# Kernel optimization log

Hardware: AMD Instinct MI355X
Metric: run time of the kernel (lower is better)

The kernel has to match this reference:

```python
import jax, jax.numpy as jnp
import numpy as np

EPS = 1e-5

def layer_norm(x, gamma, beta):
    mu = jnp.mean(x, axis=-1, keepdims=True)
    var = jnp.mean(jnp.square(x - mu), axis=-1, keepdims=True)
    return (x - mu) * jax.lax.rsqrt(var + EPS) * gamma + beta

def setup_inputs() -> dict:
    key = jax.random.key(0)
    ks = jax.random.split(key, 16)
    B, Cq, Hq, Wq = 8, 256, 32, 32
    Cc, Hc, Wc = 512, 64, 64
    def lin(k, fan_in, fan_out):
        lim = 1.0 / np.sqrt(fan_in)
        k1, k2 = jax.random.split(k)
        W = jax.random.uniform(k1, (fan_in, fan_out), jnp.float32, -lim, lim)
        b = jax.random.uniform(k2, (fan_out,), jnp.float32, -lim, lim)
        return W, b
    Wq_, bq = lin(ks[0], Cq, Cq)
    Wk_, bk = lin(ks[1], Cc, Cq)
    Wv_, bv = lin(ks[2], Cc, Cq)
    Wo_, bo = lin(ks[3], Cq, Cq)
    return {
        "query": jax.random.normal(ks[4], (B, Cq, Hq, Wq), jnp.float32),
        "context": jax.random.normal(ks[5], (B, Cc, Hc, Wc), jnp.float32),
        "Wq": Wq_, "bq": bq, "Wk": Wk_, "bk": bk, "Wv": Wv_, "bv": bv,
        "Wo": Wo_, "bo": bo,
        "gq": jnp.ones((Cq,), jnp.float32), "betq": jnp.zeros((Cq,), jnp.float32),
        "gc": jnp.ones((Cc,), jnp.float32), "betc": jnp.zeros((Cc,), jnp.float32),
    }

def reference(query, context, Wq, bq, Wk, bk, Wv, bv, Wo, bo, gq, betq, gc, betc):
    B, Cq, Hq, Wq_sp = query.shape
    _, Cc, Hc, Wc = context.shape
    num_heads = 8
    head_dim = Cq // num_heads
    scale = jnp.sqrt(jnp.float32(head_dim))
    N = Hq * Wq_sp
    # adaptive_avg_pool2d with divisible sizes == average pooling over equal bins
    ctx = context.reshape(B, Cc, Hq, Hc // Hq, Wq_sp, Wc // Wq_sp).mean(axis=(3, 5))
    q_flat = query.reshape(B, Cq, N).transpose(0, 2, 1)          # (B,N,Cq)
    c_flat = ctx.reshape(B, Cc, N).transpose(0, 2, 1)            # (B,N,Cc)
    qn = layer_norm(q_flat, gq, betq)
    cn = layer_norm(c_flat, gc, betc)
    q = (qn @ Wq + bq).reshape(B, N, num_heads, head_dim).transpose(0, 2, 1, 3)
    k = (cn @ Wk + bk).reshape(B, N, num_heads, head_dim).transpose(0, 2, 1, 3)
    v = (cn @ Wv + bv).reshape(B, N, num_heads, head_dim).transpose(0, 2, 1, 3)
    attn = jnp.einsum('bhnd,bhmd->bhnm', q, k) / scale
    attn = jax.nn.softmax(attn, axis=-1)
    out = jnp.einsum('bhnm,bhmd->bhnd', attn, v)
    out = out.transpose(0, 2, 1, 3).reshape(B, N, Cq)
    out = out @ Wo + bo
    out = q_flat + out                                           # residual
    return out.transpose(0, 2, 1).reshape(B, Cq, Hq, Wq_sp)
```

## Files before the change

kernel.cpp:

```cpp
#include <hip/hip_runtime.h>
#include <hip/hip_bf16.h>
#include <cstddef>

#define B_  8
#define CQ  256
#define CC  512
#define N_  1024
#define HQ  32
#define WQ  32
#define NH  8
#define HD  32

typedef __bf16 bf16x8 __attribute__((ext_vector_type(8)));
typedef float f32x4 __attribute__((ext_vector_type(4)));
typedef float f32x16 __attribute__((ext_vector_type(16)));
typedef unsigned int uint4v __attribute__((ext_vector_type(4)));
typedef unsigned short ushort8 __attribute__((ext_vector_type(8)));
typedef unsigned short ushort4v __attribute__((ext_vector_type(4)));

__device__ __forceinline__ unsigned short f2bf(float x) {
    return __builtin_bit_cast(unsigned short, __float2bfloat16(x));
}
__device__ __forceinline__ bf16x8 ldb8(const unsigned short* p) {
    return __builtin_bit_cast(bf16x8, *(const ushort8*)p);
}

__global__ __launch_bounds__(256) void prep_k(
    const float* __restrict__ query, const float* __restrict__ context,
    const float* __restrict__ Wq, const float* __restrict__ Wk,
    const float* __restrict__ Wv, const float* __restrict__ Wo,
    const float* __restrict__ gq, const float* __restrict__ betq,
    const float* __restrict__ gc, const float* __restrict__ betc,
    __hip_bfloat16* __restrict__ Wqt, __hip_bfloat16* __restrict__ Wkt,
    __hip_bfloat16* __restrict__ Wvt, __hip_bfloat16* __restrict__ Wot,
    __hip_bfloat16* __restrict__ qn, __hip_bfloat16* __restrict__ cn) {
    __shared__ float T[32][33];
    __shared__ float SsA[64][16];
    __shared__ float S2A[64][16];
    __shared__ float SsB[16][64];
    __shared__ float S2B[16][64];
    __shared__ float Mu[64], Rs[64];

    const int bid = blockIdx.x;
    const int tid = threadIdx.x;

    if (bid < 512) {
        const int x = bid & 15, y = (bid >> 4) & 7, z = bid >> 7;
        const float* W; __hip_bfloat16* Wt; int K;
        switch (z) {
            case 0: W = Wq; Wt = Wqt; K = CQ; break;
            case 1: W = Wk; Wt = Wkt; K = CC; break;
            case 2: W = Wv; Wt = Wvt; K = CC; break;
            default: W = Wo; Wt = Wot; K = CQ; break;
        }
        const int k0 = x * 32;
        if (k0 >= K) return;
        const int c0 = y * 32;
        const int tx = tid & 31, ty = tid >> 5;
        #pragma unroll
        for (int i = 0; i < 4; ++i) {
            const int r = ty + 8 * i;
            T[r][tx] = W[(size_t)(k0 + r) * CQ + c0 + tx];
        }
        __syncthreads();
        #pragma unroll
        for (int i = 0; i < 4; ++i) {
            const int r = ty + 8 * i;
            Wt[(size_t)(c0 + r) * K + k0 + tx] = __float2bfloat16(T[tx][r]);
        }
    } else if (bid < 1536) {
        const int u   = bid - 512;
        const int wq8 = u & 3, hq = (u >> 2) & 31, b = u >> 7;
        const int pp  = tid & 3;
        const int cg  = tid >> 2;
        const int ch0 = cg * 8;

        const float* Cb = context + ((size_t)b * CC + ch0) * 4096
                        + (size_t)(2 * hq) * 64 + (16 * wq8 + 4 * pp);
        float pv0[8], pv1[8];
        float ss0 = 0.f, ss1 = 0.f, s20 = 0.f, s21 = 0.f;
        #pragma unroll
        for (int i = 0; i < 8; ++i) {
            const float4 r0 = *(const float4*)(Cb + (size_t)i * 4096);
            const float4 r1 = *(const float4*)(Cb + (size_t)i * 4096 + 64);
            const float v0 = (r0.x + r0.y + r1.x + r1.y) * 0.25f;
            const float v1 = (r0.z + r0.w + r1.z + r1.w) * 0.25f;
            pv0[i] = v0; pv1[i] = v1;
            ss0 += v0; s20 += v0 * v0;
            ss1 += v1; s21 += v1 * v1;
        }
        SsA[cg][2 * pp]     = ss0; S2A[cg][2 * pp]     = s20;
        SsA[cg][2 * pp + 1] = ss1; S2A[cg][2 * pp + 1] = s21;
        __syncthreads();
        if (tid < 8) {
            float ts = 0.f, t2 = 0.f;
            #pragma unroll
            for (int i = 0; i < 64; ++i) { ts += SsA[i][tid]; t2 += S2A[i][tid]; }
            const float mu  = ts * (1.f / CC);
            const float var = t2 * (1.f / CC) - mu * mu;
            Mu[tid] = mu; Rs[tid] = rsqrtf(var + 1e-5f);
        }
        __syncthreads();
        const float mu0 = Mu[2 * pp],     rs0 = Rs[2 * pp];
        const float mu1 = Mu[2 * pp + 1], rs1 = Rs[2 * pp + 1];
        const int pos = hq * 32 + wq8 * 8 + 2 * pp;
        unsigned short* dst = (unsigned short*)cn
            + ((size_t)b * N_ + pos) * CC + ch0;
        ushort8 o0, o1;
        #pragma unroll
        for (int e = 0; e < 8; ++e) {
            o0[e] = f2bf((pv0[e] - mu0) * rs0 * gc[ch0 + e] + betc[ch0 + e]);
            o1[e] = f2bf((pv1[e] - mu1) * rs1 * gc[ch0 + e] + betc[ch0 + e]);
        }
        *(ushort8*)(dst)      = o0;
        *(ushort8*)(dst + CC) = o1;
    } else {
        const int u  = bid - 1536;
        const int nt = u & 15, b = u >> 4;
        const int nq = tid & 15;
        const int cg = tid >> 4;
        const int ch0 = cg * 16;
        const int nb  = nt * 64 + 4 * nq;

        const float* Qb = query + ((size_t)b * CQ + ch0) * N_ + nb;
        float qv[64];
        float ps[4] = {0.f, 0.f, 0.f, 0.f};
        float p2[4] = {0.f, 0.f, 0.f, 0.f};
        #pragma unroll
        for (int i = 0; i < 16; ++i) {
            const float4 v = *(const float4*)(Qb + (size_t)i * N_);
            qv[4 * i + 0] = v.x; qv[4 * i + 1] = v.y;
            qv[4 * i + 2] = v.z; qv[4 * i + 3] = v.w;
            ps[0] += v.x; p2[0] += v.x * v.x;
            ps[1] += v.y; p2[1] += v.y * v.y;
            ps[2] += v.z; p2[2] += v.z * v.z;
            ps[3] += v.w; p2[3] += v.w * v.w;
        }
        #pragma unroll
        for (int j = 0; j < 4; ++j) {
            SsB[cg][4 * nq + j] = ps[j];
            S2B[cg][4 * nq + j] = p2[j];
        }
        __syncthreads();
        if (tid < 64) {
            float ts = 0.f, t2 = 0.f;
            #pragma unroll
            for (int i = 0; i < 16; ++i) { ts += SsB[i][tid]; t2 += S2B[i][tid]; }
            const float mu  = ts * (1.f / CQ);
            const float var = t2 * (1.f / CQ) - mu * mu;
            Mu[tid] = mu; Rs[tid] = rsqrtf(var + 1e-5f);
        }
        __syncthreads();
        #pragma unroll
        for (int j = 0; j < 4; ++j) {
            const float mu = Mu[4 * nq + j], rs = Rs[4 * nq + j];
            ushort8 o0, o1;
            #pragma unroll
            for (int i = 0; i < 8; ++i)
                o0[i] = f2bf((qv[4 * i + j] - mu) * rs * gq[ch0 + i] + betq[ch0 + i]);
            #pragma unroll
            for (int i = 0; i < 8; ++i)
                o1[i] = f2bf((qv[4 * (8 + i) + j] - mu) * rs * gq[ch0 + 8 + i] + betq[ch0 + 8 + i]);
            unsigned short* dst = (unsigned short*)qn
                + ((size_t)b * N_ + nb + j) * CQ + ch0;
            *(ushort8*)(dst)     = o0;
            *(ushort8*)(dst + 8) = o1;
        }
    }
}

__global__ __launch_bounds__(256) void proj_all_k(
    const __hip_bfloat16* __restrict__ qn, const __hip_bfloat16* __restrict__ cn,
    const __hip_bfloat16* __restrict__ Wqt, const __hip_bfloat16* __restrict__ Wkt,
    const __hip_bfloat16* __restrict__ Wvt,
    const float* __restrict__ bq, const float* __restrict__ bk,
    const float* __restrict__ bv,
    __hip_bfloat16* __restrict__ Qb, __hip_bfloat16* __restrict__ Kb,
    __hip_bfloat16* __restrict__ Vt, float qsc) {
    __shared__ unsigned short As[64][40];
    __shared__ unsigned short B1[64][40];
    __shared__ unsigned short B2[64][40];

    const int zz = blockIdx.z;
    const int n0 = blockIdx.x * 64;
    const int c0 = blockIdx.y * 64;
    const int tid = threadIdx.x;
    const int wid = tid >> 6, lane = tid & 63;
    const int lg = lane >> 4, ln = lane & 15;
    const int wn0 = (wid & 1) * 32, wc0 = (wid >> 1) * 32;
    const int sr = tid >> 2;
    const int sk = (tid & 3) * 8;

    if (zz >= 8) {
        const int b = zz - 8;
        const unsigned short* Ab = (const unsigned short*)qn + ((size_t)b * N_ + n0) * CQ;
        const unsigned short* Wb = (const unsigned short*)Wqt + (size_t)c0 * CQ;
        f32x4 acc[2][2] = {};
        ushort8 ra = *(const ushort8*)(Ab + (size_t)sr * CQ + sk);
        ushort8 rw = *(const ushort8*)(Wb + (size_t)sr * CQ + sk);
        for (int t = 0; t < 8; ++t) {
            *(ushort8*)&As[sr][sk] = ra;
            *(ushort8*)&B1[sr][sk] = rw;
            __syncthreads();
            if (t < 7) {
                ra = *(const ushort8*)(Ab + (size_t)sr * CQ + (t + 1) * 32 + sk);
                rw = *(const ushort8*)(Wb + (size_t)sr * CQ + (t + 1) * 32 + sk);
            }
            bf16x8 a[2], w[2];
            #pragma unroll
            for (int i = 0; i < 2; ++i) a[i] = ldb8(&As[wn0 + 16 * i + ln][8 * lg]);
            #pragma unroll
            for (int j = 0; j < 2; ++j) w[j] = ldb8(&B1[wc0 + 16 * j + ln][8 * lg]);
            #pragma unroll
            for (int i = 0; i < 2; ++i)
                #pragma unroll
                for (int j = 0; j < 2; ++j)
                    acc[i][j] = __builtin_amdgcn_mfma_f32_16x16x32_bf16(a[i], w[j], acc[i][j], 0, 0, 0);
            __syncthreads();
        }
        #pragma unroll
        for (int j = 0; j < 2; ++j) {
            const int co = c0 + wc0 + 16 * j + ln;
            const int h = co >> 5, d = co & 31;
            const float bb = bq[co];
            #pragma unroll
            for (int i = 0; i < 2; ++i)
                #pragma unroll
                for (int r = 0; r < 4; ++r) {
                    const int n = n0 + wn0 + 16 * i + 4 * lg + r;
                    Qb[(((size_t)b * NH + h) * N_ + n) * HD + d] =
                        __float2bfloat16((acc[i][j][r] + bb) * qsc);
                }
        }
    } else {
        const int b = zz;
        const unsigned short* Ab  = (const unsigned short*)cn + ((size_t)b * N_ + n0) * CC;
        const unsigned short* Wkb = (const unsigned short*)Wkt + (size_t)c0 * CC;
        const unsigned short* Wvb = (const unsigned short*)Wvt + (size_t)c0 * CC;
        f32x4 accK[2][2] = {};
        f32x4 accV[2][2] = {};
        ushort8 ra = *(const ushort8*)(Ab  + (size_t)sr * CC + sk);
        ushort8 rk = *(const ushort8*)(Wkb + (size_t)sr * CC + sk);
        ushort8 rv = *(const ushort8*)(Wvb + (size_t)sr * CC + sk);
        for (int t = 0; t < 16; ++t) {
            *(ushort8*)&As[sr][sk] = ra;
            *(ushort8*)&B1[sr][sk] = rk;
            *(ushort8*)&B2[sr][sk] = rv;
            __syncthreads();
            if (t < 15) {
                ra = *(const ushort8*)(Ab  + (size_t)sr * CC + (t + 1) * 32 + sk);
                rk = *(const ushort8*)(Wkb + (size_t)sr * CC + (t + 1) * 32 + sk);
                rv = *(const ushort8*)(Wvb + (size_t)sr * CC + (t + 1) * 32 + sk);
            }
            bf16x8 a[2], wk[2], wv[2];
            #pragma unroll
            for (int i = 0; i < 2; ++i) {
                a[i]  = ldb8(&As[wn0 + 16 * i + ln][8 * lg]);
                wk[i] = ldb8(&B1[wc0 + 16 * i + ln][8 * lg]);
                wv[i] = ldb8(&B2[wc0 + 16 * i + ln][8 * lg]);
            }
            #pragma unroll
            for (int i = 0; i < 2; ++i)
                #pragma unroll
                for (int j = 0; j < 2; ++j) {
                    accK[i][j] = __builtin_amdgcn_mfma_f32_16x16x32_bf16(a[i], wk[j], accK[i][j], 0, 0, 0);
                    accV[i][j] = __builtin_amdgcn_mfma_f32_16x16x32_bf16(a[i], wv[j], accV[i][j], 0, 0, 0);
                }
            __syncthreads();
        }
        #pragma unroll
        for (int j = 0; j < 2; ++j) {
            const int co = c0 + wc0 + 16 * j + ln;
            const int h = co >> 5, d = co & 31;
            const float bbk = bk[co], bbv = bv[co];
            #pragma unroll
            for (int i = 0; i < 2; ++i) {
                const int nb = n0 + wn0 + 16 * i + 4 * lg;
                #pragma unroll
                for (int r = 0; r < 4; ++r)
                    Kb[(((size_t)b * NH + h) * N_ + nb + r) * HD + d] =
                        __float2bfloat16(accK[i][j][r] + bbk);
                ushort4v o;
                #pragma unroll
                for (int r = 0; r < 4; ++r) o[r] = f2bf(accV[i][j][r] + bbv);
                const int g  = (nb >> 2) & 3;
                const int gp = ((g & 1) << 1) | (g >> 1);
                const int nbp = (nb & ~15) | (gp << 2);
                *(ushort4v*)((unsigned short*)Vt + (((size_t)b * NH + h) * HD + d) * N_ + nbp) = o;
            }
        }
    }
}

__global__ __launch_bounds__(256) void attn32_k(
    const __hip_bfloat16* __restrict__ Q,
    const __hip_bfloat16* __restrict__ K,
    const __hip_bfloat16* __restrict__ Vt,
    __hip_bfloat16* __restrict__ O) {
    __shared__ float accS[3][64][20];
    __shared__ float lwS[3][64];

    const int lin = blockIdx.x + 32 * blockIdx.y;
    const int eff = (lin & 7) * 256 + (lin >> 3);
    const int qt  = eff & 31;
    const int bh  = eff >> 5;
    const int b   = bh >> 3;
    const int h   = bh & 7;
    const int wid  = threadIdx.x >> 6;
    const int lane = threadIdx.x & 63;
    const int l31  = lane & 31;
    const int hh   = lane >> 5;
    const int q0   = qt * 32;

    const unsigned short* Qp = (const unsigned short*)Q + ((size_t)bh * N_ + q0) * HD;
    const unsigned short* Kbb = (const unsigned short*)K + (size_t)bh * N_ * HD;
    const unsigned short* Vb = (const unsigned short*)Vt + ((size_t)bh * HD + l31) * N_;

    bf16x8 qB[2];
    #pragma unroll
    for (int m = 0; m < 2; ++m)
        qB[m] = ldb8(Qp + (size_t)l31 * HD + 16 * m + 8 * hh);

    const f32x16 Z = {0.f,0.f,0.f,0.f,0.f,0.f,0.f,0.f,
                      0.f,0.f,0.f,0.f,0.f,0.f,0.f,0.f};
    f32x16 acc = Z;
    float ls0 = 0.f, ls1 = 0.f, ls2 = 0.f, ls3 = 0.f;

    const int kvbase = wid * 256;
    const unsigned short* kp = Kbb + (size_t)(kvbase + l31) * HD + 8 * hh;
    const unsigned short* vp = Vb + kvbase + 8 * hh;

    bf16x8 kaA[2][4];
    #pragma unroll
    for (int j = 0; j < 4; ++j)
        kaA[0][j] = ldb8(kp + (j >> 1) * 1024 + (j & 1) * 16);

    #pragma unroll
    for (int st = 0; st < 4; ++st) {
        const int cur = st & 1;
        bf16x8 va[4];
        #pragma unroll
        for (int j = 0; j < 4; ++j)
            va[j] = ldb8(vp + st * 64 + 16 * j);
        if (st < 3) {
            const unsigned short* kp2 = kp + (size_t)(st + 1) * 2048;
            #pragma unroll
            for (int j = 0; j < 4; ++j)
                kaA[cur ^ 1][j] = ldb8(kp2 + (j >> 1) * 1024 + (j & 1) * 16);
        }

        f32x16 s0, s1;
        s0 = __builtin_amdgcn_mfma_f32_32x32x16_bf16(kaA[cur][0], qB[0], Z, 0, 0, 0);
        s0 = __builtin_amdgcn_mfma_f32_32x32x16_bf16(kaA[cur][1], qB[1], s0, 0, 0, 0);
        s1 = __builtin_amdgcn_mfma_f32_32x32x16_bf16(kaA[cur][2], qB[0], Z, 0, 0, 0);
        s1 = __builtin_amdgcn_mfma_f32_32x32x16_bf16(kaA[cur][3], qB[1], s1, 0, 0, 0);

        unsigned int pk[2][4][2];
        #pragma unroll
        for (int T = 0; T < 2; ++T) {
            float p[16];
            #pragma unroll
            for (int r = 0; r < 16; ++r)
                p[r] = __builtin_amdgcn_exp2f(T == 0 ? s0[r] : s1[r]);
            #pragma unroll
            for (int r = 0; r < 16; r += 4) {
                ls0 += p[r]; ls1 += p[r + 1]; ls2 += p[r + 2]; ls3 += p[r + 3];
            }
            #pragma unroll
            for (int c = 0; c < 4; ++c) {
                asm("v_cvt_pk_bf16_f32 %0, %1, %2"
                    : "=v"(pk[T][c][0]) : "v"(p[4 * c]), "v"(p[4 * c + 1]));
                asm("v_cvt_pk_bf16_f32 %0, %1, %2"
                    : "=v"(pk[T][c][1]) : "v"(p[4 * c + 2]), "v"(p[4 * c + 3]));
            }
        }

        #pragma unroll
        for (int w = 0; w < 4; ++w) {
            const int T = w >> 1, cp = w & 1;
            uint4v fu = {pk[T][2 * cp][0], pk[T][2 * cp][1],
                         pk[T][2 * cp + 1][0], pk[T][2 * cp + 1][1]};
            const bf16x8 pa = __builtin_bit_cast(bf16x8, fu);
            acc = __builtin_amdgcn_mfma_f32_32x32x16_bf16(pa, va[w], acc, 0, 0, 0);
        }
    }

    const float lsum = (ls0 + ls1) + (ls2 + ls3);
    const float lw = lsum + __shfl_xor(lsum, 32);

    if (wid > 0) {
        #pragma unroll
        for (int r4 = 0; r4 < 4; ++r4) {
            float4 v = {acc[4 * r4], acc[4 * r4 + 1], acc[4 * r4 + 2], acc[4 * r4 + 3]};
            *(float4*)&accS[wid - 1][lane][4 * r4] = v;
        }
        lwS[wid - 1][lane] = lw;
    }
    __syncthreads();
    if (wid == 0) {
        const float ltot = lw + lwS[0][lane] + lwS[1][lane] + lwS[2][lane];
        const float linv = 1.0f / ltot;
        #pragma unroll
        for (int r = 0; r < 16; ++r) {
            const int ql = (r & 3) + 8 * (r >> 2) + 4 * hh;
            const float vv = (acc[r] + accS[0][lane][r] + accS[1][lane][r]
                              + accS[2][lane][r]) * __shfl(linv, ql);
            O[((size_t)b * N_ + q0 + ql) * CQ + h * HD + l31] = __float2bfloat16(vv);
        }
    }
}

__global__ __launch_bounds__(256) void out_proj_k(const __hip_bfloat16* __restrict__ Ob,
                              const __hip_bfloat16* __restrict__ Wot,
                              const float* __restrict__ bo,
                              const float* __restrict__ query,
                              float* __restrict__ out) {
    __shared__ unsigned short As[64][40];
    __shared__ unsigned short Bs[64][40];
    const int b  = blockIdx.z;
    const int n0 = blockIdx.x * 64;
    const int c0 = blockIdx.y * 64;
    const int tid = threadIdx.x;
    const int wid = tid >> 6, lane = tid & 63;
    const int lg = lane >> 4, ln = lane & 15;
    const int wn0 = (wid & 1) * 32, wc0 = (wid >> 1) * 32;

    const unsigned short* Ab = (const unsigned short*)Ob + ((size_t)b * N_ + n0) * CQ;
    const unsigned short* Wb = (const unsigned short*)Wot + (size_t)c0 * CQ;
    const int sr = tid >> 2;
    const int sk = (tid & 3) * 8;

    f32x4 acc[2][2] = {};
    ushort8 ra = *(const ushort8*)(Ab + (size_t)sr * CQ + sk);
    ushort8 rw = *(const ushort8*)(Wb + (size_t)sr * CQ + sk);

    for (int t = 0; t < 8; ++t) {
        *(ushort8*)&As[sr][sk] = ra;
        *(ushort8*)&Bs[sr][sk] = rw;
        __syncthreads();
        if (t < 7) {
            ra = *(const ushort8*)(Ab + (size_t)sr * CQ + (t + 1) * 32 + sk);
            rw = *(const ushort8*)(Wb + (size_t)sr * CQ + (t + 1) * 32 + sk);
        }
        bf16x8 a[2], w[2];
        #pragma unroll
        for (int i = 0; i < 2; ++i)
            a[i] = ldb8(&As[wn0 + 16 * i + ln][8 * lg]);
        #pragma unroll
        for (int j = 0; j < 2; ++j)
            w[j] = ldb8(&Bs[wc0 + 16 * j + ln][8 * lg]);
        #pragma unroll
        for (int i = 0; i < 2; ++i)
            #pragma unroll
            for (int j = 0; j < 2; ++j)
                acc[i][j] = __builtin_amdgcn_mfma_f32_16x16x32_bf16(a[i], w[j], acc[i][j], 0, 0, 0);
        __syncthreads();
    }

    #pragma unroll
    for (int j = 0; j < 2; ++j) {
        const int co = c0 + wc0 + 16 * j + ln;
        const float bb = bo[co];
        #pragma unroll
        for (int i = 0; i < 2; ++i) {
            const int nb = n0 + wn0 + 16 * i + 4 * lg;
            const float4 res = *(const float4*)&query[((size_t)b * CQ + co) * N_ + nb];
            float4 o;
            o.x = acc[i][j][0] + bb + res.x;
            o.y = acc[i][j][1] + bb + res.y;
            o.z = acc[i][j][2] + bb + res.z;
            o.w = acc[i][j][3] + bb + res.w;
            *(float4*)&out[((size_t)b * CQ + co) * N_ + nb] = o;
        }
    }
}

extern "C" void kernel_launch(void* const* d_in, const int* in_sizes, int n_in,
                              void* d_out, int out_size, void* d_ws, size_t ws_size,
                              hipStream_t stream) {
    const float* query   = (const float*)d_in[0];
    const float* context = (const float*)d_in[1];
    const float* Wq = (const float*)d_in[2];
    const float* bq = (const float*)d_in[3];
    const float* Wk = (const float*)d_in[4];
    const float* bk = (const float*)d_in[5];
    const float* Wv = (const float*)d_in[6];
    const float* bv = (const float*)d_in[7];
    const float* Wo = (const float*)d_in[8];
    const float* bo = (const float*)d_in[9];
    const float* gq   = (const float*)d_in[10];
    const float* betq = (const float*)d_in[11];
    const float* gc   = (const float*)d_in[12];
    const float* betc = (const float*)d_in[13];
    float* out = (float*)d_out;

    char* w = (char*)d_ws;
    __hip_bfloat16* qn  = (__hip_bfloat16*)w;  w += (size_t)B_ * N_ * CQ * 2;
    __hip_bfloat16* cn  = (__hip_bfloat16*)w;  w += (size_t)B_ * N_ * CC * 2;
    __hip_bfloat16* Qb  = (__hip_bfloat16*)w;  w += (size_t)B_ * NH * N_ * HD * 2;
    __hip_bfloat16* Kb  = (__hip_bfloat16*)w;  w += (size_t)B_ * NH * N_ * HD * 2;
    __hip_bfloat16* Vt  = (__hip_bfloat16*)w;  w += (size_t)B_ * NH * HD * N_ * 2;
    __hip_bfloat16* Ob  = (__hip_bfloat16*)w;  w += (size_t)B_ * N_ * CQ * 2;
    __hip_bfloat16* Wqt = (__hip_bfloat16*)w;  w += (size_t)CQ * CQ * 2;
    __hip_bfloat16* Wkt = (__hip_bfloat16*)w;  w += (size_t)CQ * CC * 2;
    __hip_bfloat16* Wvt = (__hip_bfloat16*)w;  w += (size_t)CQ * CC * 2;
    __hip_bfloat16* Wot = (__hip_bfloat16*)w;  w += (size_t)CQ * CQ * 2;

    prep_k<<<dim3(1664), 256, 0, stream>>>(query, context, Wq, Wk, Wv, Wo,
                                           gq, betq, gc, betc,
                                           Wqt, Wkt, Wvt, Wot, qn, cn);

    const float qsc = 0.17677669529663687f * 1.4426950408889634f;
    proj_all_k<<<dim3(16, 4, 16), 256, 0, stream>>>(qn, cn, Wqt, Wkt, Wvt,
                                                    bq, bk, bv, Qb, Kb, Vt, qsc);

    attn32_k<<<dim3(32, 64), 256, 0, stream>>>(Qb, Kb, Vt, Ob);

    out_proj_k<<<dim3(16, 4, 8), 256, 0, stream>>>(Ob, Wot, bo, query, out);
}
```

Before: 76.73 us.

## Defer LayerNorm application into projection GEMM using precomputed row statistics

```diff
diff --git a/kernel.cpp b/kernel.cpp
--- a/kernel.cpp
+++ b/kernel.cpp
@@ -11,6 +11,10 @@
 #define NH  8
 #define HD  32
 
+#define GS_CTXS2 16384
+#define GS_QS    32768
+#define GS_QS2   40960
+
 typedef __bf16 bf16x8 __attribute__((ext_vector_type(8)));
 typedef float f32x4 __attribute__((ext_vector_type(4)));
 typedef float f32x16 __attribute__((ext_vector_type(16)));
@@ -21,6 +25,9 @@
 __device__ __forceinline__ unsigned short f2bf(float x) {
     return __builtin_bit_cast(unsigned short, __float2bfloat16(x));
 }
+__device__ __forceinline__ float bf2f(unsigned short x) {
+    return __bfloat162float(__builtin_bit_cast(__hip_bfloat16, x));
+}
 __device__ __forceinline__ bf16x8 ldb8(const unsigned short* p) {
     return __builtin_bit_cast(bf16x8, *(const ushort8*)p);
 }
@@ -29,17 +36,15 @@
     const float* __restrict__ query, const float* __restrict__ context,
     const float* __restrict__ Wq, const float* __restrict__ Wk,
     const float* __restrict__ Wv, const float* __restrict__ Wo,
-    const float* __restrict__ gq, const float* __restrict__ betq,
-    const float* __restrict__ gc, const float* __restrict__ betc,
     __hip_bfloat16* __restrict__ Wqt, __hip_bfloat16* __restrict__ Wkt,
     __hip_bfloat16* __restrict__ Wvt, __hip_bfloat16* __restrict__ Wot,
-    __hip_bfloat16* __restrict__ qn, __hip_bfloat16* __restrict__ cn) {
+    __hip_bfloat16* __restrict__ qn, __hip_bfloat16* __restrict__ cn,
+    float* __restrict__ gstats) {
     __shared__ float T[32][33];
-    __shared__ float SsA[64][16];
-    __shared__ float S2A[64][16];
+    __shared__ float SsA[32][16];
+    __shared__ float S2A[32][16];
     __shared__ float SsB[16][64];
     __shared__ float S2B[16][64];
-    __shared__ float Mu[64], Rs[64];
 
     const int bid = blockIdx.x;
     const int tid = threadIdx.x;
@@ -69,14 +74,14 @@
             Wt[(size_t)(c0 + r) * K + k0 + tx] = __float2bfloat16(T[tx][r]);
         }
     } else if (bid < 1536) {
-        const int u   = bid - 512;
-        const int wq8 = u & 3, hq = (u >> 2) & 31, b = u >> 7;
-        const int pp  = tid & 3;
-        const int cg  = tid >> 2;
-        const int ch0 = cg * 8;
+        const int u    = bid - 512;
+        const int chH  = u & 1, wqc2 = (u >> 1) & 1, hq = (u >> 2) & 31, b = u >> 7;
+        const int pp   = tid & 7;
+        const int cg   = tid >> 3;
+        const int ch0  = chH * 256 + cg * 8;
 
         const float* Cb = context + ((size_t)b * CC + ch0) * 4096
-                        + (size_t)(2 * hq) * 64 + (16 * wq8 + 4 * pp);
+                        + (size_t)(2 * hq) * 64 + (32 * wqc2 + 4 * pp);
         float pv0[8], pv1[8];
         float ss0 = 0.f, ss1 = 0.f, s20 = 0.f, s21 = 0.f;
         #pragma unroll
@@ -91,29 +96,26 @@
         }
         SsA[cg][2 * pp]     = ss0; S2A[cg][2 * pp]     = s20;
         SsA[cg][2 * pp + 1] = ss1; S2A[cg][2 * pp + 1] = s21;
-        __syncthreads();
-        if (tid < 8) {
-            float ts = 0.f, t2 = 0.f;
-            #pragma unroll
-            for (int i = 0; i < 64; ++i) { ts += SsA[i][tid]; t2 += S2A[i][tid]; }
-            const float mu  = ts * (1.f / CC);
-            const float var = t2 * (1.f / CC) - mu * mu;
-            Mu[tid] = mu; Rs[tid] = rsqrtf(var + 1e-5f);
-        }
-        __syncthreads();
-        const float mu0 = Mu[2 * pp],     rs0 = Rs[2 * pp];
-        const float mu1 = Mu[2 * pp + 1], rs1 = Rs[2 * pp + 1];
-        const int pos = hq * 32 + wq8 * 8 + 2 * pp;
+
+        const int pos0 = hq * 32 + wqc2 * 16 + 2 * pp;
         unsigned short* dst = (unsigned short*)cn
-            + ((size_t)b * N_ + pos) * CC + ch0;
+            + ((size_t)b * N_ + pos0) * CC + ch0;
         ushort8 o0, o1;
         #pragma unroll
-        for (int e = 0; e < 8; ++e) {
-            o0[e] = f2bf((pv0[e] - mu0) * rs0 * gc[ch0 + e] + betc[ch0 + e]);
-            o1[e] = f2bf((pv1[e] - mu1) * rs1 * gc[ch0 + e] + betc[ch0 + e]);
-        }
+        for (int i = 0; i < 8; ++i) { o0[i] = f2bf(pv0[i]); o1[i] = f2bf(pv1[i]); }
         *(ushort8*)(dst)      = o0;
         *(ushort8*)(dst + CC) = o1;
+
+        __syncthreads();
+        if (tid < 16) {
+            float ts = 0.f, t2 = 0.f;
+            #pragma unroll
+            for (int i = 0; i < 32; ++i) { ts += SsA[i][tid]; t2 += S2A[i][tid]; }
+            const int pos = hq * 32 + wqc2 * 16 + tid;
+            const size_t sidx = ((size_t)b * N_ + pos) * 2 + chH;
+            gstats[sidx]            = ts;
+            gstats[GS_CTXS2 + sidx] = t2;
+        }
     } else {
         const int u  = bid - 1536;
         const int nt = u & 15, b = u >> 4;
@@ -141,30 +143,28 @@
             SsB[cg][4 * nq + j] = ps[j];
             S2B[cg][4 * nq + j] = p2[j];
         }
-        __syncthreads();
-        if (tid < 64) {
-            float ts = 0.f, t2 = 0.f;
-            #pragma unroll
-            for (int i = 0; i < 16; ++i) { ts += SsB[i][tid]; t2 += S2B[i][tid]; }
-            const float mu  = ts * (1.f / CQ);
-            const float var = t2 * (1.f / CQ) - mu * mu;
-            Mu[tid] = mu; Rs[tid] = rsqrtf(var + 1e-5f);
-        }
-        __syncthreads();
+
         #pragma unroll
         for (int j = 0; j < 4; ++j) {
-            const float mu = Mu[4 * nq + j], rs = Rs[4 * nq + j];
             ushort8 o0, o1;
             #pragma unroll
-            for (int i = 0; i < 8; ++i)
-                o0[i] = f2bf((qv[4 * i + j] - mu) * rs * gq[ch0 + i] + betq[ch0 + i]);
-            #pragma unroll
-            for (int i = 0; i < 8; ++i)
-                o1[i] = f2bf((qv[4 * (8 + i) + j] - mu) * rs * gq[ch0 + 8 + i] + betq[ch0 + 8 + i]);
+            for (int i = 0; i < 8; ++i) o0[i] = f2bf(qv[4 * i + j]);
+            #pragma unroll
+            for (int i = 0; i < 8; ++i) o1[i] = f2bf(qv[4 * (8 + i) + j]);
             unsigned short* dst = (unsigned short*)qn
                 + ((size_t)b * N_ + nb + j) * CQ + ch0;
             *(ushort8*)(dst)     = o0;
             *(ushort8*)(dst + 8) = o1;
+        }
+
+        __syncthreads();
+        if (tid < 64) {
+            float ts = 0.f, t2 = 0.f;
+            #pragma unroll
+            for (int i = 0; i < 16; ++i) { ts += SsB[i][tid]; t2 += S2B[i][tid]; }
+            const size_t qidx = (size_t)b * N_ + nt * 64 + tid;
+            gstats[GS_QS  + qidx] = ts;
+            gstats[GS_QS2 + qidx] = t2;
         }
     }
 }
@@ -175,6 +175,9 @@
     const __hip_bfloat16* __restrict__ Wvt,
     const float* __restrict__ bq, const float* __restrict__ bk,
     const float* __restrict__ bv,
+    const float* __restrict__ gq, const float* __restrict__ betq,
+    const float* __restrict__ gc, const float* __restrict__ betc,
+    const float* __restrict__ gstats,
     __hip_bfloat16* __restrict__ Qb, __hip_bfloat16* __restrict__ Kb,
     __hip_bfloat16* __restrict__ Vt, float qsc) {
     __shared__ unsigned short As[64][40];
@@ -193,13 +196,33 @@
 
     if (zz >= 8) {
         const int b = zz - 8;
+        const int row = n0 + sr;
+        const float Ssum  = gstats[GS_QS  + (size_t)b * N_ + row];
+        const float S2sum = gstats[GS_QS2 + (size_t)b * N_ + row];
+        const float mu = Ssum * (1.f / CQ);
+        const float rs = rsqrtf(S2sum * (1.f / CQ) - mu * mu + 1e-5f);
+
         const unsigned short* Ab = (const unsigned short*)qn + ((size_t)b * N_ + n0) * CQ;
         const unsigned short* Wb = (const unsigned short*)Wqt + (size_t)c0 * CQ;
         f32x4 acc[2][2] = {};
         ushort8 ra = *(const ushort8*)(Ab + (size_t)sr * CQ + sk);
         ushort8 rw = *(const ushort8*)(Wb + (size_t)sr * CQ + sk);
         for (int t = 0; t < 8; ++t) {
-            *(ushort8*)&As[sr][sk] = ra;
+            const int kof = t * 32 + sk;
+            const float4 g0 = *(const float4*)&gq[kof];
+            const float4 g1 = *(const float4*)&gq[kof + 4];
+            const float4 e0 = *(const float4*)&betq[kof];
+            const float4 e1 = *(const float4*)&betq[kof + 4];
+            ushort8 st;
+            st[0] = f2bf((bf2f(ra[0]) - mu) * rs * g0.x + e0.x);
+            st[1] = f2bf((bf2f(ra[1]) - mu) * rs * g0.y + e0.y);
+            st[2] = f2bf((bf2f(ra[2]) - mu) * rs * g0.z + e0.z);
+            st[3] = f2bf((bf2f(ra[3]) - mu) * rs * g0.w + e0.w);
+            st[4] = f2bf((bf2f(ra[4]) - mu) * rs * g1.x + e1.x);
+            st[5] = f2bf((bf2f(ra[5]) - mu) * rs * g1.y + e1.y);
+            st[6] = f2bf((bf2f(ra[6]) - mu) * rs * g1.z + e1.z);
+            st[7] = f2bf((bf2f(ra[7]) - mu) * rs * g1.w + e1.w);
+            *(ushort8*)&As[sr][sk] = st;
             *(ushort8*)&B1[sr][sk] = rw;
             __syncthreads();
             if (t < 7) {
@@ -234,6 +257,13 @@
         }
     } else {
         const int b = zz;
+        const int row = n0 + sr;
+        const size_t sidx = ((size_t)b * N_ + row) * 2;
+        const float Ssum  = gstats[sidx] + gstats[sidx + 1];
+        const float S2sum = gstats[GS_CTXS2 + sidx] + gstats[GS_CTXS2 + sidx + 1];
+        const float mu = Ssum * (1.f / CC);
+        const float rs = rsqrtf(S2sum * (1.f / CC) - mu * mu + 1e-5f);
+
         const unsigned short* Ab  = (const unsigned short*)cn + ((size_t)b * N_ + n0) * CC;
         const unsigned short* Wkb = (const unsigned short*)Wkt + (size_t)c0 * CC;
         const unsigned short* Wvb = (const unsigned short*)Wvt + (size_t)c0 * CC;
@@ -243,7 +273,21 @@
         ushort8 rk = *(const ushort8*)(Wkb + (size_t)sr * CC + sk);
         ushort8 rv = *(const ushort8*)(Wvb + (size_t)sr * CC + sk);
         for (int t = 0; t < 16; ++t) {
-            *(ushort8*)&As[sr][sk] = ra;
+            const int kof = t * 32 + sk;
+            const float4 g0 = *(const float4*)&gc[kof];
+            const float4 g1 = *(const float4*)&gc[kof + 4];
+            const float4 e0 = *(const float4*)&betc[kof];
+            const float4 e1 = *(const float4*)&betc[kof + 4];
+            ushort8 st;
+            st[0] = f2bf((bf2f(ra[0]) - mu) * rs * g0.x + e0.x);
+            st[1] = f2bf((bf2f(ra[1]) - mu) * rs * g0.y + e0.y);
+            st[2] = f2bf((bf2f(ra[2]) - mu) * rs * g0.z + e0.z);
+            st[3] = f2bf((bf2f(ra[3]) - mu) * rs * g0.w + e0.w);
+            st[4] = f2bf((bf2f(ra[4]) - mu) * rs * g1.x + e1.x);
+            st[5] = f2bf((bf2f(ra[5]) - mu) * rs * g1.y + e1.y);
+            st[6] = f2bf((bf2f(ra[6]) - mu) * rs * g1.z + e1.z);
+            st[7] = f2bf((bf2f(ra[7]) - mu) * rs * g1.w + e1.w);
+            *(ushort8*)&As[sr][sk] = st;
             *(ushort8*)&B1[sr][sk] = rk;
             *(ushort8*)&B2[sr][sk] = rv;
             __syncthreads();
@@ -505,14 +549,16 @@
     __hip_bfloat16* Wkt = (__hip_bfloat16*)w;  w += (size_t)CQ * CC * 2;
     __hip_bfloat16* Wvt = (__hip_bfloat16*)w;  w += (size_t)CQ * CC * 2;
     __hip_bfloat16* Wot = (__hip_bfloat16*)w;  w += (size_t)CQ * CQ * 2;
+    float* gstats = (float*)w;                 w += (size_t)49152 * 4;
 
     prep_k<<<dim3(1664), 256, 0, stream>>>(query, context, Wq, Wk, Wv, Wo,
-                                           gq, betq, gc, betc,
-                                           Wqt, Wkt, Wvt, Wot, qn, cn);
+                                           Wqt, Wkt, Wvt, Wot, qn, cn, gstats);
 
     const float qsc = 0.17677669529663687f * 1.4426950408889634f;
     proj_all_k<<<dim3(16, 4, 16), 256, 0, stream>>>(qn, cn, Wqt, Wkt, Wvt,
-                                                    bq, bk, bv, Qb, Kb, Vt, qsc);
+                                                    bq, bk, bv,
+                                                    gq, betq, gc, betc, gstats,
+                                                    Qb, Kb, Vt, qsc);
 
     attn32_k<<<dim3(32, 64), 256, 0, stream>>>(Qb, Kb, Vt, Ob);
 
```

Measured after the change: 70.30 us. 1.09x faster.
